# Performance work log

Hardware: AMD Instinct MI355X
Metric: run time of the kernel (lower is better)

## Reference

```python
import jax, jax.numpy as jnp
import numpy as np
import math


def _sinusoidal_pe(seq_len, hidden_dim, dtype):
    pos = jnp.arange(seq_len, dtype=jnp.float32)[:, None]              # [S,1]
    div = jnp.exp(jnp.arange(0, hidden_dim, 2, dtype=jnp.float32) * (-math.log(10000.0) / hidden_dim))  # [H/2]
    ang = pos * div                                                    # [S,H/2]
    pe = jnp.stack([jnp.sin(ang), jnp.cos(ang)], axis=-1).reshape(seq_len, hidden_dim)  # interleave sin/cos
    return pe.astype(dtype)


def setup_inputs() -> dict:
    key = jax.random.key(0)
    ks = jax.random.split(key, 12)
    B, S, H = 4, 2048, 1024
    scale = 1.0 / math.sqrt(H)
    inp = {
        "x": jax.random.normal(ks[0], (B, S, H), dtype=jnp.float32),
        "mask": jax.random.randint(ks[1], (B, S, S), 0, 2, dtype=jnp.int32),
        "Wq": jax.random.normal(ks[2], (H, H), dtype=jnp.float32) * scale,
        "bq": jax.random.normal(ks[3], (H,), dtype=jnp.float32) * 0.02,
        "Wk": jax.random.normal(ks[4], (H, H), dtype=jnp.float32) * scale,
        "bk": jax.random.normal(ks[5], (H,), dtype=jnp.float32) * 0.02,
        "Wv": jax.random.normal(ks[6], (H, H), dtype=jnp.float32) * scale,
        "bv": jax.random.normal(ks[7], (H,), dtype=jnp.float32) * 0.02,
        "pos_bias": jax.random.normal(ks[8], (S, S), dtype=jnp.float32),
        "Wo": jax.random.normal(ks[9], (H, H), dtype=jnp.float32) * scale,
        "bo": jax.random.normal(ks[10], (H,), dtype=jnp.float32) * 0.02,
        "gamma": jnp.ones((H,), dtype=jnp.float32),
        "beta": jnp.zeros((H,), dtype=jnp.float32),
    }
    return inp


def reference(x, mask, Wq, bq, Wk, bk, Wv, bv, pos_bias, Wo, bo, gamma, beta):
    B, S, H = x.shape
    scale = math.sqrt(H)
    pe = _sinusoidal_pe(S, H, x.dtype)                  # [S,H]
    xp = x + pe[None, :, :]                             # [B,S,H]
    # torch Linear: y = x @ W.T + b
    q = jnp.einsum('bsh,oh->bso', xp, Wq) + bq
    k = jnp.einsum('bsh,oh->bso', xp, Wk) + bk
    v = jnp.einsum('bsh,oh->bso', xp, Wv) + bv
    scores = jnp.einsum('bqh,bkh->bqk', q, k) / scale   # [B,S,S]
    scores = scores + pos_bias[None, :S, :S]
    scores = jnp.where(mask == 0, jnp.asarray(-1e9, scores.dtype), scores)
    attn = jax.nn.softmax(scores, axis=-1)              # dropout = identity (eval mode)
    context = jnp.einsum('bqk,bkh->bqh', attn, v)
    out = jnp.einsum('bsh,oh->bso', context, Wo) + bo
    # LayerNorm(out + x)
    h = out + x
    mu = jnp.mean(h, axis=-1, keepdims=True)
    var = jnp.var(h, axis=-1, keepdims=True)
    normed = (h - mu) * jax.lax.rsqrt(var + 1e-5) * gamma + beta
    return normed, attn
```

## Files before the change

### kernel.cpp

```cpp
#include <hip/hip_runtime.h>
#include <hip/hip_bf16.h>
#include <math.h>

typedef __hip_bfloat16 bf16;
typedef __bf16 bf16x8 __attribute__((ext_vector_type(8)));
typedef float f32x4 __attribute__((ext_vector_type(4)));

static constexpr int  B_  = 4, S_ = 2048, H_ = 1024;
static constexpr long BSH = (long)B_ * S_ * H_;
static constexpr long SH  = (long)S_ * H_;
static constexpr long SS  = (long)S_ * S_;
static constexpr long HH  = (long)H_ * H_;

#define GLOAD_LDS16(gp, lp)                                                          \
  __builtin_amdgcn_global_load_lds((__attribute__((address_space(1))) void*)(gp),    \
                                   (__attribute__((address_space(3))) void*)(lp),    \
                                   16, 0, 0)

#define BARRIER() do { __builtin_amdgcn_s_barrier(); asm volatile("" ::: "memory"); } while (0)

template <int N> __device__ __forceinline__ void waitcnt_vm() {
  if constexpr (N == 0)      asm volatile("s_waitcnt vmcnt(0)" ::: "memory");
  else if constexpr (N == 8) asm volatile("s_waitcnt vmcnt(8)" ::: "memory");
}

__device__ __forceinline__ float wave_reduce_sum(float v) {
#pragma unroll
  for (int o = 32; o; o >>= 1) v += __shfl_xor(v, o, 64);
  return v;
}
__device__ __forceinline__ float bf16r(float v) {
  return __bfloat162float(__float2bfloat16(v));
}

__global__ void prep_kernel(const float* __restrict__ Wq, const float* __restrict__ Wk,
                            const float* __restrict__ Wv, const float* __restrict__ Wo,
                            bf16* __restrict__ wdst,
                            const float* __restrict__ x, bf16* __restrict__ xpb,
                            const int* __restrict__ mask, unsigned* __restrict__ mask_bits) {
  const int bx  = blockIdx.x;
  const int tid = threadIdx.x;
  if (bx < 4096) {
    const int w = bx >> 10;
    const float* src = (w == 0) ? Wq : (w == 1) ? Wk : (w == 2) ? Wv : Wo;
    bf16* d = wdst + (long)w * HH;
    const int idx = ((bx & 1023) << 8) + tid;
    const float4 f = ((const float4*)src)[idx];
    d[idx * 4 + 0] = __float2bfloat16(f.x);
    d[idx * 4 + 1] = __float2bfloat16(f.y);
    d[idx * 4 + 2] = __float2bfloat16(f.z);
    d[idx * 4 + 3] = __float2bfloat16(f.w);
  } else if (bx < 20480) {
    const long idx = (((long)(bx - 4096)) << 8) + tid;
    const int  i   = (int)(idx & (H_ / 2 - 1));
    const long bs  = idx >> 9;
    const int  s   = (int)(bs & (S_ - 1));
    const float div = __expf((float)(2 * i) * (-9.210340371976184f / (float)H_));
    const float ang = (float)s * div;
    const float2 xv = ((const float2*)x)[idx];
    xpb[idx * 2 + 0] = __float2bfloat16(xv.x + __sinf(ang));
    xpb[idx * 2 + 1] = __float2bfloat16(xv.y + __cosf(ang));
  } else {
    const long uidx = (((long)(bx - 20480)) << 8) + tid;
    const int4* mp  = (const int4*)mask + uidx * 8;
    unsigned bits = 0;
#pragma unroll
    for (int q = 0; q < 8; ++q) {
      const int4 v = mp[q];
      bits |= (v.x ? 1u : 0u) << (q * 4 + 0);
      bits |= (v.y ? 1u : 0u) << (q * 4 + 1);
      bits |= (v.z ? 1u : 0u) << (q * 4 + 2);
      bits |= (v.w ? 1u : 0u) << (q * 4 + 3);
    }
    mask_bits[uidx] = bits;
  }
}

template <int MODE, bool DBUF>
__global__ void gemm_nt(const bf16* __restrict__ A, long sA,
                        const bf16* __restrict__ Bm, long sB,
                        bf16* __restrict__ Cb, float* __restrict__ Cf, long sC,
                        int M, int N, int K,
                        const float* __restrict__ bias0,
                        const float* __restrict__ bias1,
                        const float* __restrict__ bias2,
                        const float* __restrict__ pos_bias,
                        const unsigned* __restrict__ mask_bits,
                        const float* __restrict__ xres,
                        const float* __restrict__ inv_sum) {
  constexpr int BM = 128, BN = 128, BK = 64;
  constexpr int NBUF = DBUF ? 2 : 1;
  __shared__ bf16 As[NBUF][BM * BK];
  __shared__ bf16 Bs[NBUF][BN * BK];

  const int tid  = threadIdx.x;
  const int lane = tid & 63;
  const int wave = tid >> 6;
  const int wm   = wave & 1;
  const int wn   = wave >> 1;
  const int z    = blockIdx.z;
  const int m0   = blockIdx.x * BM;
  const int n0   = blockIdx.y * BN;

  const bf16* Ab = A  + (long)z * sA;
  const bf16* Bb = Bm + (long)z * sB;

  const int rw = tid >> 3;
  const int cp = (tid & 7) ^ (rw & 7);
  const bf16* ga = Ab + (long)(m0 + rw) * K + cp * 8;
  const bf16* gb = Bb + (long)(n0 + rw) * K + cp * 8;

  auto stage = [&](int tile, int buf) {
    const long k0 = (long)tile * BK;
#pragma unroll
    for (int q = 0; q < 4; ++q) {
      GLOAD_LDS16(ga + (long)(32 * q) * K + k0, &As[buf][tid * 8 + q * 2048]);
      GLOAD_LDS16(gb + (long)(32 * q) * K + k0, &Bs[buf][tid * 8 + q * 2048]);
    }
  };

  f32x4 acc[4][4] = {};

  const int fr     = lane & 15;
  const int k0slot = lane >> 4;
  const int sw     = fr & 7;

  auto tile_compute = [&](const char* bAc, const char* bBc) {
#pragma unroll
    for (int ks = 0; ks < 2; ++ks) {
      const int co = ((k0slot + 4 * ks) ^ sw) << 4;
      bf16x8 af[4], bfv[4];
#pragma unroll
      for (int i = 0; i < 4; ++i) {
        af[i]  = *(const bf16x8*)(bAc + (wm * 64 + i * 16 + fr) * 128 + co);
        bfv[i] = *(const bf16x8*)(bBc + (wn * 64 + i * 16 + fr) * 128 + co);
      }
#pragma unroll
      for (int i = 0; i < 4; ++i)
#pragma unroll
        for (int j = 0; j < 4; ++j)
          acc[i][j] = __builtin_amdgcn_mfma_f32_16x16x32_bf16(af[i], bfv[j], acc[i][j], 0, 0, 0);
    }
  };

  const int nkt = K / BK;
  if constexpr (DBUF) {
    stage(0, 0);
    for (int kt = 0; kt < nkt; ++kt) {
      const int cur = kt & 1;
      if (kt + 1 < nkt) {
        stage(kt + 1, (cur ^ 1) & (NBUF - 1));
        waitcnt_vm<8>();
      } else {
        waitcnt_vm<0>();
      }
      BARRIER();
      tile_compute((const char*)&As[cur][0], (const char*)&Bs[cur][0]);
      BARRIER();
    }
  } else {
    for (int kt = 0; kt < nkt; ++kt) {
      stage(kt, 0);
      __syncthreads();
      tile_compute((const char*)&As[0][0], (const char*)&Bs[0][0]);
      __syncthreads();
    }
  }

  const float* biasz = (MODE == 0) ? ((z == 0) ? bias0 : bias1) : bias0;

  const int cc = lane & 15;
  const int cr = (lane >> 4) * 4;
#pragma unroll
  for (int i = 0; i < 4; ++i) {
    const int rowb = m0 + wm * 64 + i * 16 + cr;
#pragma unroll
    for (int j = 0; j < 4; ++j) {
      const int col = n0 + wn * 64 + j * 16 + cc;
#pragma unroll
      for (int r = 0; r < 4; ++r) {
        const int  row  = rowb + r;
        const long loff = (long)row * N + col;
        const long off  = (long)z * sC + loff;
        const float v   = acc[i][j][r];
        if (MODE == 0) {
          Cb[off] = __float2bfloat16(v + biasz[col]);
        } else if (MODE == 1) {
          const unsigned mw = mask_bits[off >> 5];
          float sc = v * (1.0f / 32.0f) + pos_bias[loff];
          if (((mw >> (col & 31)) & 1u) == 0u) sc = -1e9f;
          Cb[off] = __float2bfloat16(__expf(fminf(sc, 60.0f)));
        } else if (MODE == 2) {
          Cb[off] = __float2bfloat16(v * inv_sum[z * S_ + row]);
        } else if (MODE == 3) {
          Cf[off] = v + biasz[col] + xres[off];
        } else {
          Cb[off] = __float2bfloat16(v + bias0[row]);
        }
      }
    }
  }
}

__global__ void rownorm_kernel(const bf16* __restrict__ E, float* __restrict__ attn_f,
                               float* __restrict__ inv_sum) {
  const long row = blockIdx.x;
  const int  tid = threadIdx.x;
  const uint4 d = *(const uint4*)(E + row * (long)S_ + tid * 8);
  float ev[8];
  ev[0] = __uint_as_float(d.x << 16); ev[1] = __uint_as_float(d.x & 0xffff0000u);
  ev[2] = __uint_as_float(d.y << 16); ev[3] = __uint_as_float(d.y & 0xffff0000u);
  ev[4] = __uint_as_float(d.z << 16); ev[5] = __uint_as_float(d.z & 0xffff0000u);
  ev[6] = __uint_as_float(d.w << 16); ev[7] = __uint_as_float(d.w & 0xffff0000u);
  float s = 0.f;
#pragma unroll
  for (int i = 0; i < 8; ++i) s += ev[i];
  s = wave_reduce_sum(s);
  __shared__ float red[4];
  if ((tid & 63) == 0) red[tid >> 6] = s;
  __syncthreads();
  const float inv = 1.0f / fmaxf(red[0] + red[1] + red[2] + red[3], 1e-30f);
  if (tid == 0) inv_sum[row] = inv;
  float4 o0, o1;
  o0.x = bf16r(ev[0] * inv); o0.y = bf16r(ev[1] * inv);
  o0.z = bf16r(ev[2] * inv); o0.w = bf16r(ev[3] * inv);
  o1.x = bf16r(ev[4] * inv); o1.y = bf16r(ev[5] * inv);
  o1.z = bf16r(ev[6] * inv); o1.w = bf16r(ev[7] * inv);
  float4* dst = (float4*)(attn_f + row * (long)S_ + tid * 8);
  dst[0] = o0;
  dst[1] = o1;
}

__global__ void ln_kernel(float* __restrict__ h, const float* __restrict__ gamma,
                          const float* __restrict__ beta) {
  const long row = blockIdx.x;
  float* hr = h + row * (long)H_;
  const int tid = threadIdx.x;
  float v[4];
  float s = 0.f;
#pragma unroll
  for (int i = 0; i < 4; ++i) { v[i] = hr[tid + i * 256]; s += v[i]; }
  s = wave_reduce_sum(s);
  __shared__ float redA[4], redB[4];
  if ((tid & 63) == 0) redA[tid >> 6] = s;
  __syncthreads();
  const float mu = (redA[0] + redA[1] + redA[2] + redA[3]) * (1.0f / H_);
  float vs = 0.f;
#pragma unroll
  for (int i = 0; i < 4; ++i) { const float d = v[i] - mu; vs += d * d; }
  vs = wave_reduce_sum(vs);
  if ((tid & 63) == 0) redB[tid >> 6] = vs;
  __syncthreads();
  const float var  = (redB[0] + redB[1] + redB[2] + redB[3]) * (1.0f / H_);
  const float rstd = rsqrtf(var + 1e-5f);
#pragma unroll
  for (int i = 0; i < 4; ++i) {
    const int c = tid + i * 256;
    hr[c] = bf16r((v[i] - mu) * rstd * gamma[c] + beta[c]);
  }
}

extern "C" void kernel_launch(void* const* d_in, const int* in_sizes, int n_in,
                              void* d_out, int out_size, void* d_ws, size_t ws_size,
                              hipStream_t stream) {
  const float* x        = (const float*)d_in[0];
  const int*   mask     = (const int*)d_in[1];
  const float* Wq       = (const float*)d_in[2];
  const float* bq       = (const float*)d_in[3];
  const float* Wk       = (const float*)d_in[4];
  const float* bk       = (const float*)d_in[5];
  const float* Wv       = (const float*)d_in[6];
  const float* bv       = (const float*)d_in[7];
  const float* pos_bias = (const float*)d_in[8];
  const float* Wo       = (const float*)d_in[9];
  const float* bo       = (const float*)d_in[10];
  const float* gamma    = (const float*)d_in[11];
  const float* beta     = (const float*)d_in[12];

  float* normed_f = (float*)d_out;
  float* attn_f   = (float*)((char*)d_out + ((size_t)32 << 20));

  const size_t MiB = (size_t)1 << 20;
  bf16*     xpb       = (bf16*)d_ws;
  bf16*     q_b       = (bf16*)((char*)d_ws +  16 * MiB);
  bf16*     kbuf      = (bf16*)((char*)d_ws +  32 * MiB);
  bf16*     vT        = (bf16*)((char*)d_ws +  64 * MiB);
  bf16*     ctx       = (bf16*)((char*)d_ws +  80 * MiB);
  bf16*     attn_b    = (bf16*)((char*)d_ws +  96 * MiB);
  bf16*     wts       = (bf16*)((char*)d_ws + 128 * MiB);
  float*    inv_sum   = (float*)((char*)d_ws + 136 * MiB);
  unsigned* mask_bits = (unsigned*)((char*)d_ws + 137 * MiB);
  bf16* Wqb = wts, *Wvb = wts + 2 * HH, *Wob = wts + 3 * HH;

  const int MQKV = B_ * S_;

  prep_kernel<<<dim3(22528), 256, 0, stream>>>(Wq, Wk, Wv, Wo, wts, x, xpb,
                                               mask, mask_bits);

  gemm_nt<0, false><<<dim3(64, 8, 2), 256, 0, stream>>>(xpb, 0, Wqb, HH, q_b, nullptr, BSH,
                                                        MQKV, H_, H_, bq, bk, nullptr,
                                                        nullptr, nullptr, nullptr, nullptr);

  gemm_nt<4, false><<<dim3(8, 16, 4), 256, 0, stream>>>(Wvb, 0, xpb, SH, vT, nullptr, SH,
                                                        H_, S_, H_, bv, nullptr, nullptr,
                                                        nullptr, nullptr, nullptr, nullptr);

  gemm_nt<1, false><<<dim3(16, 16, B_), 256, 0, stream>>>(q_b, SH, kbuf, SH,
                                                          attn_b, nullptr, SS,
                                                          S_, S_, H_, nullptr, nullptr, nullptr,
                                                          pos_bias, mask_bits, nullptr, nullptr);

  rownorm_kernel<<<B_ * S_, 256, 0, stream>>>(attn_b, attn_f, inv_sum);

  gemm_nt<2, true><<<dim3(16, 8, B_), 256, 0, stream>>>(attn_b, SS, vT, SH,
                                                        ctx, nullptr, SH,
                                                        S_, H_, S_, nullptr, nullptr, nullptr,
                                                        nullptr, nullptr, nullptr, inv_sum);

  gemm_nt<3, false><<<dim3(64, 8, 1), 256, 0, stream>>>(ctx, 0, Wob, 0, nullptr, normed_f, 0,
                                                        MQKV, H_, H_, bo, nullptr, nullptr,
                                                        nullptr, nullptr, x, nullptr);

  ln_kernel<<<B_ * S_, 256, 0, stream>>>(normed_f, gamma, beta);
}
```

Before: 421.0 us.

## Pre-convert pos_bias to bf16, fold score scale into Q, vectorize LayerNorm

Adds a prep stage that converts pos_bias to bf16 so the score GEMM epilogue reads half the bytes, and folds the 1/sqrt(H) scale into the Q projection epilogue. It also rewrites the LayerNorm kernel to use float4 loads and stores. Rounding pos_bias and the pre-scaled Q to bf16 changes numerics slightly, and the extra conversion pass adds traffic in the prep kernel.

```diff
diff --git a/kernel.cpp b/kernel.cpp
--- a/kernel.cpp
+++ b/kernel.cpp
@@ -37,7 +37,8 @@
                             const float* __restrict__ Wv, const float* __restrict__ Wo,
                             bf16* __restrict__ wdst,
                             const float* __restrict__ x, bf16* __restrict__ xpb,
-                            const int* __restrict__ mask, unsigned* __restrict__ mask_bits) {
+                            const int* __restrict__ mask, unsigned* __restrict__ mask_bits,
+                            const float* __restrict__ pos_bias, bf16* __restrict__ pbb) {
   const int bx  = blockIdx.x;
   const int tid = threadIdx.x;
   if (bx < 4096) {
@@ -60,7 +61,7 @@
     const float2 xv = ((const float2*)x)[idx];
     xpb[idx * 2 + 0] = __float2bfloat16(xv.x + __sinf(ang));
     xpb[idx * 2 + 1] = __float2bfloat16(xv.y + __cosf(ang));
-  } else {
+  } else if (bx < 22528) {
     const long uidx = (((long)(bx - 20480)) << 8) + tid;
     const int4* mp  = (const int4*)mask + uidx * 8;
     unsigned bits = 0;
@@ -73,6 +74,14 @@
       bits |= (v.w ? 1u : 0u) << (q * 4 + 3);
     }
     mask_bits[uidx] = bits;
+  } else {
+    const long idx = (((long)(bx - 22528)) << 8) + tid;
+    const float4 f = ((const float4*)pos_bias)[idx];
+    bf16* d = pbb + idx * 4;
+    d[0] = __float2bfloat16(f.x);
+    d[1] = __float2bfloat16(f.y);
+    d[2] = __float2bfloat16(f.z);
+    d[3] = __float2bfloat16(f.w);
   }
 }
 
@@ -84,7 +93,7 @@
                         const float* __restrict__ bias0,
                         const float* __restrict__ bias1,
                         const float* __restrict__ bias2,
-                        const float* __restrict__ pos_bias,
+                        const bf16* __restrict__ pos_bias,
                         const unsigned* __restrict__ mask_bits,
                         const float* __restrict__ xres,
                         const float* __restrict__ inv_sum) {
@@ -184,10 +193,12 @@
         const long off  = (long)z * sC + loff;
         const float v   = acc[i][j][r];
         if (MODE == 0) {
-          Cb[off] = __float2bfloat16(v + biasz[col]);
+          float o = v + biasz[col];
+          if (z == 0) o *= 0.03125f;
+          Cb[off] = __float2bfloat16(o);
         } else if (MODE == 1) {
           const unsigned mw = mask_bits[off >> 5];
-          float sc = v * (1.0f / 32.0f) + pos_bias[loff];
+          float sc = v + __bfloat162float(pos_bias[loff]);
           if (((mw >> (col & 31)) & 1u) == 0u) sc = -1e9f;
           Cb[off] = __float2bfloat16(__expf(fminf(sc, 60.0f)));
         } else if (MODE == 2) {
@@ -236,28 +247,28 @@
   const long row = blockIdx.x;
   float* hr = h + row * (long)H_;
   const int tid = threadIdx.x;
-  float v[4];
-  float s = 0.f;
-#pragma unroll
-  for (int i = 0; i < 4; ++i) { v[i] = hr[tid + i * 256]; s += v[i]; }
+  const float4 v4 = ((const float4*)hr)[tid];
+  float s = v4.x + v4.y + v4.z + v4.w;
   s = wave_reduce_sum(s);
   __shared__ float redA[4], redB[4];
   if ((tid & 63) == 0) redA[tid >> 6] = s;
   __syncthreads();
   const float mu = (redA[0] + redA[1] + redA[2] + redA[3]) * (1.0f / H_);
-  float vs = 0.f;
-#pragma unroll
-  for (int i = 0; i < 4; ++i) { const float d = v[i] - mu; vs += d * d; }
+  const float dx = v4.x - mu, dy = v4.y - mu, dz = v4.z - mu, dw = v4.w - mu;
+  float vs = dx * dx + dy * dy + dz * dz + dw * dw;
   vs = wave_reduce_sum(vs);
   if ((tid & 63) == 0) redB[tid >> 6] = vs;
   __syncthreads();
   const float var  = (redB[0] + redB[1] + redB[2] + redB[3]) * (1.0f / H_);
   const float rstd = rsqrtf(var + 1e-5f);
-#pragma unroll
-  for (int i = 0; i < 4; ++i) {
-    const int c = tid + i * 256;
-    hr[c] = bf16r((v[i] - mu) * rstd * gamma[c] + beta[c]);
-  }
+  const float4 g4 = ((const float4*)gamma)[tid];
+  const float4 b4 = ((const float4*)beta)[tid];
+  float4 o;
+  o.x = bf16r(dx * rstd * g4.x + b4.x);
+  o.y = bf16r(dy * rstd * g4.y + b4.y);
+  o.z = bf16r(dz * rstd * g4.z + b4.z);
+  o.w = bf16r(dw * rstd * g4.w + b4.w);
+  ((float4*)hr)[tid] = o;
 }
 
 extern "C" void kernel_launch(void* const* d_in, const int* in_sizes, int n_in,
@@ -290,12 +301,13 @@
   bf16*     wts       = (bf16*)((char*)d_ws + 128 * MiB);
   float*    inv_sum   = (float*)((char*)d_ws + 136 * MiB);
   unsigned* mask_bits = (unsigned*)((char*)d_ws + 137 * MiB);
+  bf16*     pbb       = (bf16*)((char*)d_ws + 139 * MiB);
   bf16* Wqb = wts, *Wvb = wts + 2 * HH, *Wob = wts + 3 * HH;
 
   const int MQKV = B_ * S_;
 
-  prep_kernel<<<dim3(22528), 256, 0, stream>>>(Wq, Wk, Wv, Wo, wts, x, xpb,
-                                               mask, mask_bits);
+  prep_kernel<<<dim3(26624), 256, 0, stream>>>(Wq, Wk, Wv, Wo, wts, x, xpb,
+                                               mask, mask_bits, pos_bias, pbb);
 
   gemm_nt<0, false><<<dim3(64, 8, 2), 256, 0, stream>>>(xpb, 0, Wqb, HH, q_b, nullptr, BSH,
                                                         MQKV, H_, H_, bq, bk, nullptr,
@@ -308,7 +320,7 @@
   gemm_nt<1, false><<<dim3(16, 16, B_), 256, 0, stream>>>(q_b, SH, kbuf, SH,
                                                           attn_b, nullptr, SS,
                                                           S_, S_, H_, nullptr, nullptr, nullptr,
-                                                          pos_bias, mask_bits, nullptr, nullptr);
+                                                          pbb, mask_bits, nullptr, nullptr);
 
   rownorm_kernel<<<B_ * S_, 256, 0, stream>>>(attn_b, attn_f, inv_sum);
 
```

Result: no change. 424.1 us (+0.7%).
